# Kernel tuning notes

Hardware: AMD Instinct MI355X
Metric: run time of the kernel (lower is better)

Reference implementation:

```python
import jax, jax.numpy as jnp
import numpy as np

N = 8192
IN_DIM = 1024
HID = 64
N_CLASS = 40
N_LAYERS = 4  # N_LAYERS-1 hidden GraphConvolutions + 1 output layer


def _row_normalize(a):
    return a / jnp.clip(a.sum(axis=1, keepdims=True), 1e-6)


def setup_inputs() -> dict:
    key = jax.random.key(0)
    ks = jax.random.split(key, 10)
    x = jax.random.normal(ks[0], (N, IN_DIM), dtype=jnp.float32)
    # symmetric-ish normalized dense adjacency surrogates
    adj1 = _row_normalize(jax.random.uniform(ks[1], (N, N), dtype=jnp.float32))
    adj2 = _row_normalize(jax.random.uniform(ks[2], (N, N), dtype=jnp.float32))
    s_in = 1.0 / np.sqrt(IN_DIM)
    s_h = 1.0 / np.sqrt(HID)
    fc1_W = jax.random.uniform(ks[3], (IN_DIM, HID), minval=-s_in, maxval=s_in)
    fc1_b = jnp.zeros((HID,), jnp.float32)
    W_h = jax.random.uniform(ks[4], (N_LAYERS - 1, HID, HID), minval=-s_h, maxval=s_h)
    b_h = jnp.zeros((N_LAYERS - 1, HID), jnp.float32)
    W_out = jax.random.uniform(ks[5], (HID, N_CLASS), minval=-s_h, maxval=s_h)
    b_out = jnp.zeros((N_CLASS,), jnp.float32)
    return {"x": x, "adj1": adj1, "adj2": adj2, "fc1_W": fc1_W, "fc1_b": fc1_b,
            "W_h": W_h, "b_h": b_h, "W_out": W_out, "b_out": b_out}


def reference(x, adj1, adj2, fc1_W, fc1_b, W_h, b_h, W_out, b_out):
    # fc1 projection (dropout is identity in eval mode)
    h = x @ fc1_W + fc1_b  # [N, HID]
    # hidden GraphConvolution layers: aggregate, bias, residual, relu
    for i in range(W_h.shape[0]):
        h = jax.nn.relu(adj1 @ (h @ W_h[i]) + b_h[i] + h)
    # final layer: no residual
    out = jax.nn.relu(adj1 @ (h @ W_out) + b_out)  # [N, N_CLASS]
    return out
```

## Files before the change

kernel.cpp:

```cpp
#include <hip/hip_runtime.h>
#include <hip/hip_bf16.h>

typedef __attribute__((ext_vector_type(8))) short short8;
typedef __attribute__((ext_vector_type(4))) float f32x4;

#define NROWS 8192
#define BK 256
#define MTILE 128
#define SK 8

__device__ inline short f2bf(float f) {
  union { float f; unsigned u; } v; v.f = f;
  unsigned r = v.u + 0x7FFFu + ((v.u >> 16) & 1u);
  return (short)(r >> 16);
}

__global__ __launch_bounds__(256) void convert_adj_kernel(
    const float* __restrict__ A, short* __restrict__ AB) {
  const size_t total = (size_t)NROWS * NROWS;
  size_t i0 = ((size_t)blockIdx.x * 256 + threadIdx.x) * 8;
  size_t stride = (size_t)gridDim.x * 256 * 8;
  for (size_t i = i0; i < total; i += stride) {
    f32x4 a = __builtin_nontemporal_load((const f32x4*)(A + i));
    f32x4 b = __builtin_nontemporal_load((const f32x4*)(A + i + 4));
    short8 o;
    o[0] = f2bf(a.x); o[1] = f2bf(a.y); o[2] = f2bf(a.z); o[3] = f2bf(a.w);
    o[4] = f2bf(b.x); o[5] = f2bf(b.y); o[6] = f2bf(b.z); o[7] = f2bf(b.w);
    *(short8*)(AB + i) = o;
  }
}

__global__ __launch_bounds__(256) void convert_w_kernel(
    const float* __restrict__ W, short* __restrict__ WT, int K, int N) {
  int gid = blockIdx.x * 256 + threadIdx.x;
  if (gid >= K * N) return;
  int n = gid / K, k = gid - n * K;
  WT[gid] = f2bf(W[(size_t)k * N + n]);
}

__global__ __launch_bounds__(256) void small_t_kernel(
    const float* __restrict__ H, const float* __restrict__ W,
    short* __restrict__ tT, int Nout, int ldw) {
  __shared__ float Ws[64][64];
  int tid = threadIdx.x;
  for (int i = tid; i < 64 * 64; i += 256) {
    int j = i >> 6, n = i & 63;
    Ws[j][n] = (n < Nout) ? W[j * ldw + n] : 0.0f;
  }
  __syncthreads();
  int gid = blockIdx.x * 256 + tid;
  int m = gid >> 2;
  int nq = (gid & 3) << 4;
  const float* hrow = H + (size_t)m * 64;
  float hr[64];
#pragma unroll
  for (int j = 0; j < 64; j += 4) {
    f32x4 v = *(const f32x4*)(hrow + j);
    hr[j] = v.x; hr[j + 1] = v.y; hr[j + 2] = v.z; hr[j + 3] = v.w;
  }
#pragma unroll
  for (int ni = 0; ni < 16; ++ni) {
    int n = nq + ni;
    float acc = 0.0f;
#pragma unroll
    for (int j = 0; j < 64; ++j) acc += hr[j] * Ws[j][n];
    tT[(size_t)n * NROWS + m] = f2bf(acc);
  }
}

__global__ __launch_bounds__(256, 2) void gemm_bf16_lds2(
    const short* __restrict__ AB, const short* __restrict__ BT,
    float* __restrict__ P) {
  __shared__ short Bs[2][64][BK + 8];
  int tid = threadIdx.x;
  int w = tid >> 6, l = tid & 63;
  int l15 = l & 15, kg = l >> 4;
  int m_base = blockIdx.x * MTILE;
  int wrow = m_base + w * 32;
  const short* A0 = AB + (size_t)(wrow + l15) * NROWS;
  const short* A1 = AB + (size_t)(wrow + 16 + l15) * NROWS;
  const int KCH = NROWS / SK;
  const int NST = KCH / BK;
  int k0 = blockIdx.y * KCH;
  f32x4 acc[2][4];
#pragma unroll
  for (int rt = 0; rt < 2; ++rt)
#pragma unroll
    for (int ct = 0; ct < 4; ++ct) acc[rt][ct] = (f32x4){0, 0, 0, 0};

  short8 st[8];
#pragma unroll
  for (int j = 0; j < 8; ++j) {
    int slot = tid + 256 * j;
    int r = slot >> 5, c = (slot & 31) << 3;
    st[j] = *(const short8*)(BT + (size_t)r * NROWS + k0 + c);
  }
#pragma unroll
  for (int j = 0; j < 8; ++j) {
    int slot = tid + 256 * j;
    int r = slot >> 5, c = (slot & 31) << 3;
    *(short8*)&Bs[0][r][c] = st[j];
  }
  __syncthreads();

  for (int t = 0; t < NST; ++t) {
    int cur = t & 1;
    if (t + 1 < NST) {
      int ks = k0 + (t + 1) * BK;
#pragma unroll
      for (int j = 0; j < 8; ++j) {
        int slot = tid + 256 * j;
        int r = slot >> 5, c = (slot & 31) << 3;
        st[j] = *(const short8*)(BT + (size_t)r * NROWS + ks + c);
      }
    }
    int ks = k0 + t * BK;
#pragma unroll
    for (int k = 0; k < BK; k += 64) {
      short8 a[2][2], b[2][4];
#pragma unroll
      for (int u = 0; u < 2; ++u) {
        int kk = k + u * 32 + kg * 8;
        a[u][0] = *(const short8*)(A0 + ks + kk);
        a[u][1] = *(const short8*)(A1 + ks + kk);
        b[u][0] = *(const short8*)&Bs[cur][l15 +  0][kk];
        b[u][1] = *(const short8*)&Bs[cur][l15 + 16][kk];
        b[u][2] = *(const short8*)&Bs[cur][l15 + 32][kk];
        b[u][3] = *(const short8*)&Bs[cur][l15 + 48][kk];
      }
#pragma unroll
      for (int u = 0; u < 2; ++u)
#pragma unroll
        for (int ct = 0; ct < 4; ++ct) {
          acc[0][ct] = __builtin_amdgcn_mfma_f32_16x16x32_bf16(a[u][0], b[u][ct], acc[0][ct], 0, 0, 0);
          acc[1][ct] = __builtin_amdgcn_mfma_f32_16x16x32_bf16(a[u][1], b[u][ct], acc[1][ct], 0, 0, 0);
        }
    }
    __syncthreads();
    if (t + 1 < NST) {
#pragma unroll
      for (int j = 0; j < 8; ++j) {
        int slot = tid + 256 * j;
        int r = slot >> 5, c = (slot & 31) << 3;
        *(short8*)&Bs[cur ^ 1][r][c] = st[j];
      }
      __syncthreads();
    }
  }

  float* Pb = P + (size_t)blockIdx.y * (NROWS * 64);
#pragma unroll
  for (int rt = 0; rt < 2; ++rt)
#pragma unroll
    for (int r = 0; r < 4; ++r) {
      size_t base = (size_t)(wrow + rt * 16 + kg * 4 + r) * 64 + l15;
#pragma unroll
      for (int ct = 0; ct < 4; ++ct) Pb[base + 16 * ct] = acc[rt][ct][r];
    }
}

__global__ __launch_bounds__(256, 2) void gemm_a32_u2(
    const float* __restrict__ A, const short* __restrict__ BT,
    float* __restrict__ P, int K, int splitk) {
  int w = threadIdx.x >> 6;
  int l = threadIdx.x & 63;
  int l15 = l & 15, kg = l >> 4;
  int m_base = blockIdx.x * 64 + w * 16;
  const float* Arow = A + (size_t)(m_base + l15) * K;
  const short* Br = BT + (size_t)l15 * K;
  int kchunk = K / splitk;
  int k0 = blockIdx.y * kchunk;
  f32x4 acc[4] = {{0,0,0,0},{0,0,0,0},{0,0,0,0},{0,0,0,0}};
  for (int k = k0; k < k0 + kchunk; k += 64) {
    f32x4 a32[2][2];
    short8 b[2][4];
#pragma unroll
    for (int u = 0; u < 2; ++u) {
      int kk = k + u * 32 + kg * 8;
      a32[u][0] = __builtin_nontemporal_load((const f32x4*)(Arow + kk));
      a32[u][1] = __builtin_nontemporal_load((const f32x4*)(Arow + kk + 4));
      b[u][0] = *(const short8*)(Br + kk);
      b[u][1] = *(const short8*)(Br + (size_t)16 * K + kk);
      b[u][2] = *(const short8*)(Br + (size_t)32 * K + kk);
      b[u][3] = *(const short8*)(Br + (size_t)48 * K + kk);
    }
#pragma unroll
    for (int u = 0; u < 2; ++u) {
      short8 af;
      af[0] = f2bf(a32[u][0].x); af[1] = f2bf(a32[u][0].y);
      af[2] = f2bf(a32[u][0].z); af[3] = f2bf(a32[u][0].w);
      af[4] = f2bf(a32[u][1].x); af[5] = f2bf(a32[u][1].y);
      af[6] = f2bf(a32[u][1].z); af[7] = f2bf(a32[u][1].w);
#pragma unroll
      for (int t = 0; t < 4; ++t)
        acc[t] = __builtin_amdgcn_mfma_f32_16x16x32_bf16(af, b[u][t], acc[t], 0, 0, 0);
    }
  }
  float* Pb = P + (size_t)blockIdx.y * (NROWS * 64);
  int mr = m_base + kg * 4;
#pragma unroll
  for (int r = 0; r < 4; ++r) {
    size_t base = (size_t)(mr + r) * 64 + l15;
#pragma unroll
    for (int t = 0; t < 4; ++t) Pb[base + 16 * t] = acc[t][r];
  }
}

__global__ __launch_bounds__(256) void reduce4_kernel(
    const float* __restrict__ P, const float* __restrict__ bias,
    const float* __restrict__ Hres, float* __restrict__ Hout,
    float* __restrict__ Out, int mode, int splitk) {
  int gid = blockIdx.x * 256 + threadIdx.x;
  int e0 = gid * 4;
  int n = e0 & 63;
  f32x4 s = {0, 0, 0, 0};
  for (int sidx = 0; sidx < splitk; ++sidx)
    s += *(const f32x4*)(P + (size_t)sidx * (NROWS * 64) + e0);
  s += *(const f32x4*)(bias + n);
  if (mode == 0) {
    *(f32x4*)(Hout + e0) = s;
  } else if (mode == 1) {
    s += *(const f32x4*)(Hres + e0);
    s.x = s.x > 0.f ? s.x : 0.f; s.y = s.y > 0.f ? s.y : 0.f;
    s.z = s.z > 0.f ? s.z : 0.f; s.w = s.w > 0.f ? s.w : 0.f;
    *(f32x4*)(Hout + e0) = s;
  } else {
    if (n < 40) {
      int m = e0 >> 6;
      s.x = s.x > 0.f ? s.x : 0.f; s.y = s.y > 0.f ? s.y : 0.f;
      s.z = s.z > 0.f ? s.z : 0.f; s.w = s.w > 0.f ? s.w : 0.f;
      *(f32x4*)(Out + (size_t)m * 40 + n) = s;
    }
  }
}

extern "C" void kernel_launch(void* const* d_in, const int* in_sizes, int n_in,
                              void* d_out, int out_size, void* d_ws, size_t ws_size,
                              hipStream_t stream) {
  const float* x     = (const float*)d_in[0];
  const float* adj1  = (const float*)d_in[1];
  const float* fc1_W = (const float*)d_in[3];
  const float* fc1_b = (const float*)d_in[4];
  const float* W_h   = (const float*)d_in[5];
  const float* b_h   = (const float*)d_in[6];
  const float* W_out = (const float*)d_in[7];
  const float* b_out = (const float*)d_in[8];
  float* out = (float*)d_out;

  char* ws = (char*)d_ws;
  size_t off = 0;
  float* P   = (float*)(ws + off); off += (size_t)SK * NROWS * 64 * 4;
  float* h_a = (float*)(ws + off); off += (size_t)NROWS * 64 * 4;
  float* h_b = (float*)(ws + off); off += (size_t)NROWS * 64 * 4;
  short* tT  = (short*)(ws + off); off += (size_t)64 * NROWS * 2;
  short* WT  = (short*)(ws + off); off += (size_t)64 * 1024 * 2;
  size_t adjb_bytes = (size_t)NROWS * NROWS * 2;
  short* AB  = (ws_size - off >= adjb_bytes) ? (short*)(ws + off) : nullptr;

  const int RED_GRID = NROWS * 64 / 4 / 256;

  if (AB)
    convert_adj_kernel<<<2048, 256, 0, stream>>>(adj1, AB);

  convert_w_kernel<<<(1024 * 64 + 255) / 256, 256, 0, stream>>>(fc1_W, WT, 1024, 64);
  gemm_a32_u2<<<dim3(NROWS / 64, SK), 256, 0, stream>>>(x, WT, P, 1024, SK);
  reduce4_kernel<<<RED_GRID, 256, 0, stream>>>(P, fc1_b, nullptr, h_a, nullptr, 0, SK);

  float* hc = h_a; float* hn = h_b;
  for (int i = 0; i < 3; ++i) {
    small_t_kernel<<<NROWS * 4 / 256, 256, 0, stream>>>(hc, W_h + (size_t)i * 64 * 64, tT, 64, 64);
    if (AB)
      gemm_bf16_lds2<<<dim3(NROWS / MTILE, SK), 256, 0, stream>>>(AB, tT, P);
    else
      gemm_a32_u2<<<dim3(NROWS / 64, SK), 256, 0, stream>>>(adj1, tT, P, NROWS, SK);
    reduce4_kernel<<<RED_GRID, 256, 0, stream>>>(P, b_h + (size_t)i * 64, hc, hn, nullptr, 1, SK);
    float* t = hc; hc = hn; hn = t;
  }

  small_t_kernel<<<NROWS * 4 / 256, 256, 0, stream>>>(hc, W_out, tT, 40, 40);
  if (AB)
    gemm_bf16_lds2<<<dim3(NROWS / MTILE, SK), 256, 0, stream>>>(AB, tT, P);
  else
    gemm_a32_u2<<<dim3(NROWS / 64, SK), 256, 0, stream>>>(adj1, tT, P, NROWS, SK);
  reduce4_kernel<<<RED_GRID, 256, 0, stream>>>(P, b_out, nullptr, nullptr, out, 2, SK);
}
```

Baseline: 252.9 us.

## Fuse adjacency bf16 conversion into first aggregation GEMM and retile to 256 rows

Removes the separate fp32-to-bf16 adjacency conversion pass and folds it into the first aggregation GEMM. That kernel reads adj1 in fp32, converts it in registers, writes the bf16 copy for later layers and uses it directly in MFMA. Both adjacency GEMMs now use 256-row tiles, with each wave holding 4x4 accumulators, BK 128 and split-K of 16 for more A reuse per B tile. The trade-offs are more registers, a larger partial-sum buffer, and reduce kernels that now sum 16 partial slices instead of 8.

```diff
diff --git a/kernel.cpp b/kernel.cpp
--- a/kernel.cpp
+++ b/kernel.cpp
@@ -5,29 +5,15 @@
 typedef __attribute__((ext_vector_type(4))) float f32x4;
 
 #define NROWS 8192
-#define BK 256
-#define MTILE 128
-#define SK 8
+#define BK 128
+#define MTILE 256
+#define SKADJ 16
+#define SKFC 8
 
 __device__ inline short f2bf(float f) {
   union { float f; unsigned u; } v; v.f = f;
   unsigned r = v.u + 0x7FFFu + ((v.u >> 16) & 1u);
   return (short)(r >> 16);
-}
-
-__global__ __launch_bounds__(256) void convert_adj_kernel(
-    const float* __restrict__ A, short* __restrict__ AB) {
-  const size_t total = (size_t)NROWS * NROWS;
-  size_t i0 = ((size_t)blockIdx.x * 256 + threadIdx.x) * 8;
-  size_t stride = (size_t)gridDim.x * 256 * 8;
-  for (size_t i = i0; i < total; i += stride) {
-    f32x4 a = __builtin_nontemporal_load((const f32x4*)(A + i));
-    f32x4 b = __builtin_nontemporal_load((const f32x4*)(A + i + 4));
-    short8 o;
-    o[0] = f2bf(a.x); o[1] = f2bf(a.y); o[2] = f2bf(a.z); o[3] = f2bf(a.w);
-    o[4] = f2bf(b.x); o[5] = f2bf(b.y); o[6] = f2bf(b.z); o[7] = f2bf(b.w);
-    *(short8*)(AB + i) = o;
-  }
 }
 
 __global__ __launch_bounds__(256) void convert_w_kernel(
@@ -68,37 +54,39 @@
   }
 }
 
-__global__ __launch_bounds__(256, 2) void gemm_bf16_lds2(
+
+__global__ __launch_bounds__(256, 2) void gemm_bf16_r4(
     const short* __restrict__ AB, const short* __restrict__ BT,
     float* __restrict__ P) {
   __shared__ short Bs[2][64][BK + 8];
   int tid = threadIdx.x;
   int w = tid >> 6, l = tid & 63;
   int l15 = l & 15, kg = l >> 4;
-  int m_base = blockIdx.x * MTILE;
-  int wrow = m_base + w * 32;
-  const short* A0 = AB + (size_t)(wrow + l15) * NROWS;
+  int wrow = blockIdx.x * MTILE + w * 64;
+  const short* A0 = AB + (size_t)(wrow +  0 + l15) * NROWS;
   const short* A1 = AB + (size_t)(wrow + 16 + l15) * NROWS;
-  const int KCH = NROWS / SK;
+  const short* A2 = AB + (size_t)(wrow + 32 + l15) * NROWS;
+  const short* A3 = AB + (size_t)(wrow + 48 + l15) * NROWS;
+  const int KCH = NROWS / SKADJ;
   const int NST = KCH / BK;
   int k0 = blockIdx.y * KCH;
-  f32x4 acc[2][4];
-#pragma unroll
-  for (int rt = 0; rt < 2; ++rt)
+  f32x4 acc[4][4];
+#pragma unroll
+  for (int rt = 0; rt < 4; ++rt)
 #pragma unroll
     for (int ct = 0; ct < 4; ++ct) acc[rt][ct] = (f32x4){0, 0, 0, 0};
 
-  short8 st[8];
-#pragma unroll
-  for (int j = 0; j < 8; ++j) {
+  short8 st[4];
+#pragma unroll
+  for (int j = 0; j < 4; ++j) {
     int slot = tid + 256 * j;
-    int r = slot >> 5, c = (slot & 31) << 3;
+    int r = slot >> 4, c = (slot & 15) << 3;
     st[j] = *(const short8*)(BT + (size_t)r * NROWS + k0 + c);
   }
 #pragma unroll
-  for (int j = 0; j < 8; ++j) {
+  for (int j = 0; j < 4; ++j) {
     int slot = tid + 256 * j;
-    int r = slot >> 5, c = (slot & 31) << 3;
+    int r = slot >> 4, c = (slot & 15) << 3;
     *(short8*)&Bs[0][r][c] = st[j];
   }
   __syncthreads();
@@ -108,40 +96,50 @@
     if (t + 1 < NST) {
       int ks = k0 + (t + 1) * BK;
 #pragma unroll
-      for (int j = 0; j < 8; ++j) {
+      for (int j = 0; j < 4; ++j) {
         int slot = tid + 256 * j;
-        int r = slot >> 5, c = (slot & 31) << 3;
+        int r = slot >> 4, c = (slot & 15) << 3;
         st[j] = *(const short8*)(BT + (size_t)r * NROWS + ks + c);
       }
     }
     int ks = k0 + t * BK;
 #pragma unroll
     for (int k = 0; k < BK; k += 64) {
-      short8 a[2][2], b[2][4];
 #pragma unroll
       for (int u = 0; u < 2; ++u) {
         int kk = k + u * 32 + kg * 8;
-        a[u][0] = *(const short8*)(A0 + ks + kk);
-        a[u][1] = *(const short8*)(A1 + ks + kk);
-        b[u][0] = *(const short8*)&Bs[cur][l15 +  0][kk];
-        b[u][1] = *(const short8*)&Bs[cur][l15 + 16][kk];
-        b[u][2] = *(const short8*)&Bs[cur][l15 + 32][kk];
-        b[u][3] = *(const short8*)&Bs[cur][l15 + 48][kk];
-      }
-#pragma unroll
-      for (int u = 0; u < 2; ++u)
-#pragma unroll
-        for (int ct = 0; ct < 4; ++ct) {
-          acc[0][ct] = __builtin_amdgcn_mfma_f32_16x16x32_bf16(a[u][0], b[u][ct], acc[0][ct], 0, 0, 0);
-          acc[1][ct] = __builtin_amdgcn_mfma_f32_16x16x32_bf16(a[u][1], b[u][ct], acc[1][ct], 0, 0, 0);
-        }
+        short8 a0 = *(const short8*)(A0 + ks + kk);
+        short8 a1 = *(const short8*)(A1 + ks + kk);
+        short8 a2 = *(const short8*)(A2 + ks + kk);
+        short8 a3 = *(const short8*)(A3 + ks + kk);
+        short8 b0 = *(const short8*)&Bs[cur][l15 +  0][kk];
+        short8 b1 = *(const short8*)&Bs[cur][l15 + 16][kk];
+        short8 b2 = *(const short8*)&Bs[cur][l15 + 32][kk];
+        short8 b3 = *(const short8*)&Bs[cur][l15 + 48][kk];
+        acc[0][0] = __builtin_amdgcn_mfma_f32_16x16x32_bf16(a0, b0, acc[0][0], 0, 0, 0);
+        acc[0][1] = __builtin_amdgcn_mfma_f32_16x16x32_bf16(a0, b1, acc[0][1], 0, 0, 0);
+        acc[0][2] = __builtin_amdgcn_mfma_f32_16x16x32_bf16(a0, b2, acc[0][2], 0, 0, 0);
+        acc[0][3] = __builtin_amdgcn_mfma_f32_16x16x32_bf16(a0, b3, acc[0][3], 0, 0, 0);
+        acc[1][0] = __builtin_amdgcn_mfma_f32_16x16x32_bf16(a1, b0, acc[1][0], 0, 0, 0);
+        acc[1][1] = __builtin_amdgcn_mfma_f32_16x16x32_bf16(a1, b1, acc[1][1], 0, 0, 0);
+        acc[1][2] = __builtin_amdgcn_mfma_f32_16x16x32_bf16(a1, b2, acc[1][2], 0, 0, 0);
+        acc[1][3] = __builtin_amdgcn_mfma_f32_16x16x32_bf16(a1, b3, acc[1][3], 0, 0, 0);
+        acc[2][0] = __builtin_amdgcn_mfma_f32_16x16x32_bf16(a2, b0, acc[2][0], 0, 0, 0);
+        acc[2][1] = __builtin_amdgcn_mfma_f32_16x16x32_bf16(a2, b1, acc[2][1], 0, 0, 0);
+        acc[2][2] = __builtin_amdgcn_mfma_f32_16x16x32_bf16(a2, b2, acc[2][2], 0, 0, 0);
+        acc[2][3] = __builtin_amdgcn_mfma_f32_16x16x32_bf16(a2, b3, acc[2][3], 0, 0, 0);
+        acc[3][0] = __builtin_amdgcn_mfma_f32_16x16x32_bf16(a3, b0, acc[3][0], 0, 0, 0);
+        acc[3][1] = __builtin_amdgcn_mfma_f32_16x16x32_bf16(a3, b1, acc[3][1], 0, 0, 0);
+        acc[3][2] = __builtin_amdgcn_mfma_f32_16x16x32_bf16(a3, b2, acc[3][2], 0, 0, 0);
+        acc[3][3] = __builtin_amdgcn_mfma_f32_16x16x32_bf16(a3, b3, acc[3][3], 0, 0, 0);
+      }
     }
     __syncthreads();
     if (t + 1 < NST) {
 #pragma unroll
-      for (int j = 0; j < 8; ++j) {
+      for (int j = 0; j < 4; ++j) {
         int slot = tid + 256 * j;
-        int r = slot >> 5, c = (slot & 31) << 3;
+        int r = slot >> 4, c = (slot & 15) << 3;
         *(short8*)&Bs[cur ^ 1][r][c] = st[j];
       }
       __syncthreads();
@@ -150,7 +148,121 @@
 
   float* Pb = P + (size_t)blockIdx.y * (NROWS * 64);
 #pragma unroll
-  for (int rt = 0; rt < 2; ++rt)
+  for (int rt = 0; rt < 4; ++rt)
+#pragma unroll
+    for (int r = 0; r < 4; ++r) {
+      size_t base = (size_t)(wrow + rt * 16 + kg * 4 + r) * 64 + l15;
+#pragma unroll
+      for (int ct = 0; ct < 4; ++ct) Pb[base + 16 * ct] = acc[rt][ct][r];
+    }
+}
+
+__global__ __launch_bounds__(256, 2) void gemm_fusedcvt_r4(
+    const float* __restrict__ A, const short* __restrict__ BT,
+    float* __restrict__ P, short* __restrict__ AB) {
+  __shared__ short Bs[2][64][BK + 8];
+  int tid = threadIdx.x;
+  int w = tid >> 6, l = tid & 63;
+  int l15 = l & 15, kg = l >> 4;
+  int wrow = blockIdx.x * MTILE + w * 64;
+  const float* F0 = A + (size_t)(wrow +  0 + l15) * NROWS;
+  const float* F1 = A + (size_t)(wrow + 16 + l15) * NROWS;
+  const float* F2 = A + (size_t)(wrow + 32 + l15) * NROWS;
+  const float* F3 = A + (size_t)(wrow + 48 + l15) * NROWS;
+  short* S0 = AB + (size_t)(wrow +  0 + l15) * NROWS;
+  short* S1 = AB + (size_t)(wrow + 16 + l15) * NROWS;
+  short* S2 = AB + (size_t)(wrow + 32 + l15) * NROWS;
+  short* S3 = AB + (size_t)(wrow + 48 + l15) * NROWS;
+  const int KCH = NROWS / SKADJ;
+  const int NST = KCH / BK;
+  int k0 = blockIdx.y * KCH;
+  f32x4 acc[4][4];
+#pragma unroll
+  for (int rt = 0; rt < 4; ++rt)
+#pragma unroll
+    for (int ct = 0; ct < 4; ++ct) acc[rt][ct] = (f32x4){0, 0, 0, 0};
+
+  short8 st[4];
+#pragma unroll
+  for (int j = 0; j < 4; ++j) {
+    int slot = tid + 256 * j;
+    int r = slot >> 4, c = (slot & 15) << 3;
+    st[j] = *(const short8*)(BT + (size_t)r * NROWS + k0 + c);
+  }
+#pragma unroll
+  for (int j = 0; j < 4; ++j) {
+    int slot = tid + 256 * j;
+    int r = slot >> 4, c = (slot & 15) << 3;
+    *(short8*)&Bs[0][r][c] = st[j];
+  }
+  __syncthreads();
+
+  for (int t = 0; t < NST; ++t) {
+    int cur = t & 1;
+    if (t + 1 < NST) {
+      int ks = k0 + (t + 1) * BK;
+#pragma unroll
+      for (int j = 0; j < 4; ++j) {
+        int slot = tid + 256 * j;
+        int r = slot >> 4, c = (slot & 15) << 3;
+        st[j] = *(const short8*)(BT + (size_t)r * NROWS + ks + c);
+      }
+    }
+    int ks = k0 + t * BK;
+#pragma unroll
+    for (int k = 0; k < BK; k += 64) {
+#pragma unroll
+      for (int u = 0; u < 2; ++u) {
+        int kk = k + u * 32 + kg * 8;
+        f32x4 f[4][2];
+        f[0][0] = __builtin_nontemporal_load((const f32x4*)(F0 + ks + kk));
+        f[0][1] = __builtin_nontemporal_load((const f32x4*)(F0 + ks + kk + 4));
+        f[1][0] = __builtin_nontemporal_load((const f32x4*)(F1 + ks + kk));
+        f[1][1] = __builtin_nontemporal_load((const f32x4*)(F1 + ks + kk + 4));
+        f[2][0] = __builtin_nontemporal_load((const f32x4*)(F2 + ks + kk));
+        f[2][1] = __builtin_nontemporal_load((const f32x4*)(F2 + ks + kk + 4));
+        f[3][0] = __builtin_nontemporal_load((const f32x4*)(F3 + ks + kk));
+        f[3][1] = __builtin_nontemporal_load((const f32x4*)(F3 + ks + kk + 4));
+        short8 a[4];
+#pragma unroll
+        for (int rt = 0; rt < 4; ++rt) {
+          a[rt][0] = f2bf(f[rt][0].x); a[rt][1] = f2bf(f[rt][0].y);
+          a[rt][2] = f2bf(f[rt][0].z); a[rt][3] = f2bf(f[rt][0].w);
+          a[rt][4] = f2bf(f[rt][1].x); a[rt][5] = f2bf(f[rt][1].y);
+          a[rt][6] = f2bf(f[rt][1].z); a[rt][7] = f2bf(f[rt][1].w);
+        }
+        *(short8*)(S0 + ks + kk) = a[0];
+        *(short8*)(S1 + ks + kk) = a[1];
+        *(short8*)(S2 + ks + kk) = a[2];
+        *(short8*)(S3 + ks + kk) = a[3];
+        short8 b0 = *(const short8*)&Bs[cur][l15 +  0][kk];
+        short8 b1 = *(const short8*)&Bs[cur][l15 + 16][kk];
+        short8 b2 = *(const short8*)&Bs[cur][l15 + 32][kk];
+        short8 b3 = *(const short8*)&Bs[cur][l15 + 48][kk];
+#pragma unroll
+        for (int rt = 0; rt < 4; ++rt) {
+          acc[rt][0] = __builtin_amdgcn_mfma_f32_16x16x32_bf16(a[rt], b0, acc[rt][0], 0, 0, 0);
+          acc[rt][1] = __builtin_amdgcn_mfma_f32_16x16x32_bf16(a[rt], b1, acc[rt][1], 0, 0, 0);
+          acc[rt][2] = __builtin_amdgcn_mfma_f32_16x16x32_bf16(a[rt], b2, acc[rt][2], 0, 0, 0);
+          acc[rt][3] = __builtin_amdgcn_mfma_f32_16x16x32_bf16(a[rt], b3, acc[rt][3], 0, 0, 0);
+        }
+      }
+    }
+    __syncthreads();
+    if (t + 1 < NST) {
+#pragma unroll
+      for (int j = 0; j < 4; ++j) {
+        int slot = tid + 256 * j;
+        int r = slot >> 4, c = (slot & 15) << 3;
+        *(short8*)&Bs[cur ^ 1][r][c] = st[j];
+      }
+      __syncthreads();
+    }
+  }
+
+  float* Pb = P + (size_t)blockIdx.y * (NROWS * 64);
+#pragma unroll
+  for (int rt = 0; rt < 4; ++rt)
 #pragma unroll
     for (int r = 0; r < 4; ++r) {
       size_t base = (size_t)(wrow + rt * 16 + kg * 4 + r) * 64 + l15;
@@ -249,7 +361,7 @@
 
   char* ws = (char*)d_ws;
   size_t off = 0;
-  float* P   = (float*)(ws + off); off += (size_t)SK * NROWS * 64 * 4;
+  float* P   = (float*)(ws + off); off += (size_t)SKADJ * NROWS * 64 * 4;
   float* h_a = (float*)(ws + off); off += (size_t)NROWS * 64 * 4;
   float* h_b = (float*)(ws + off); off += (size_t)NROWS * 64 * 4;
   short* tT  = (short*)(ws + off); off += (size_t)64 * NROWS * 2;
@@ -259,28 +371,29 @@
 
   const int RED_GRID = NROWS * 64 / 4 / 256;
 
-  if (AB)
-    convert_adj_kernel<<<2048, 256, 0, stream>>>(adj1, AB);
-
   convert_w_kernel<<<(1024 * 64 + 255) / 256, 256, 0, stream>>>(fc1_W, WT, 1024, 64);
-  gemm_a32_u2<<<dim3(NROWS / 64, SK), 256, 0, stream>>>(x, WT, P, 1024, SK);
-  reduce4_kernel<<<RED_GRID, 256, 0, stream>>>(P, fc1_b, nullptr, h_a, nullptr, 0, SK);
+  gemm_a32_u2<<<dim3(NROWS / 64, SKFC), 256, 0, stream>>>(x, WT, P, 1024, SKFC);
+  reduce4_kernel<<<RED_GRID, 256, 0, stream>>>(P, fc1_b, nullptr, h_a, nullptr, 0, SKFC);
 
   float* hc = h_a; float* hn = h_b;
   for (int i = 0; i < 3; ++i) {
     small_t_kernel<<<NROWS * 4 / 256, 256, 0, stream>>>(hc, W_h + (size_t)i * 64 * 64, tT, 64, 64);
-    if (AB)
-      gemm_bf16_lds2<<<dim3(NROWS / MTILE, SK), 256, 0, stream>>>(AB, tT, P);
-    else
-      gemm_a32_u2<<<dim3(NROWS / 64, SK), 256, 0, stream>>>(adj1, tT, P, NROWS, SK);
-    reduce4_kernel<<<RED_GRID, 256, 0, stream>>>(P, b_h + (size_t)i * 64, hc, hn, nullptr, 1, SK);
+    if (AB) {
+      if (i == 0)
+        gemm_fusedcvt_r4<<<dim3(NROWS / MTILE, SKADJ), 256, 0, stream>>>(adj1, tT, P, AB);
+      else
+        gemm_bf16_r4<<<dim3(NROWS / MTILE, SKADJ), 256, 0, stream>>>(AB, tT, P);
+    } else {
+      gemm_a32_u2<<<dim3(NROWS / 64, SKADJ), 256, 0, stream>>>(adj1, tT, P, NROWS, SKADJ);
+    }
+    reduce4_kernel<<<RED_GRID, 256, 0, stream>>>(P, b_h + (size_t)i * 64, hc, hn, nullptr, 1, SKADJ);
     float* t = hc; hc = hn; hn = t;
   }
 
   small_t_kernel<<<NROWS * 4 / 256, 256, 0, stream>>>(hc, W_out, tT, 40, 40);
   if (AB)
-    gemm_bf16_lds2<<<dim3(NROWS / MTILE, SK), 256, 0, stream>>>(AB, tT, P);
+    gemm_bf16_r4<<<dim3(NROWS / MTILE, SKADJ), 256, 0, stream>>>(AB, tT, P);
   else
-    gemm_a32_u2<<<dim3(NROWS / 64, SK), 256, 0, stream>>>(adj1, tT, P, NROWS, SK);
-  reduce4_kernel<<<RED_GRID, 256, 0, stream>>>(P, b_out, nullptr, nullptr, out, 2, SK);
-}
+    gemm_a32_u2<<<dim3(NROWS / 64, SKADJ), 256, 0, stream>>>(adj1, tT, P, NROWS, SKADJ);
+  reduce4_kernel<<<RED_GRID, 256, 0, stream>>>(P, b_out, nullptr, nullptr, out, 2, SKADJ);
+}
```

Result: slower. 274.5 us (+8.5%).

## Enlarge adjacency GEMM to 64-row warp tiles, bf16 fc1 path, split-K 16

Applied to the files above, without the earlier changes.

The adjacency GEMM now has each warp cover 64 rows, with 4x4 MFMA tiles and 256-row blocks, so every LDS B fragment is reused across four A row tiles. Split-K rises to 16 to keep the grid large with the bigger tiles, which doubles the partial-sum traffic through the reduce kernels. The input x is also converted to bf16 so the fc1 projection can run on the same templated bf16 GEMM. The extra conversion pass and the higher register pressure from 64 accumulators per lane are the tradeoffs.

```diff
diff --git a/kernel.cpp b/kernel.cpp
--- a/kernel.cpp
+++ b/kernel.cpp
@@ -5,9 +5,9 @@
 typedef __attribute__((ext_vector_type(4))) float f32x4;
 
 #define NROWS 8192
-#define BK 256
-#define MTILE 128
-#define SK 8
+#define MTILE 256
+#define SKADJ 16
+#define SKFC 8
 
 __device__ inline short f2bf(float f) {
   union { float f; unsigned u; } v; v.f = f;
@@ -15,9 +15,8 @@
   return (short)(r >> 16);
 }
 
-__global__ __launch_bounds__(256) void convert_adj_kernel(
-    const float* __restrict__ A, short* __restrict__ AB) {
-  const size_t total = (size_t)NROWS * NROWS;
+__global__ __launch_bounds__(256) void convert_f32_kernel(
+    const float* __restrict__ A, short* __restrict__ O, size_t total) {
   size_t i0 = ((size_t)blockIdx.x * 256 + threadIdx.x) * 8;
   size_t stride = (size_t)gridDim.x * 256 * 8;
   for (size_t i = i0; i < total; i += stride) {
@@ -26,7 +25,7 @@
     short8 o;
     o[0] = f2bf(a.x); o[1] = f2bf(a.y); o[2] = f2bf(a.z); o[3] = f2bf(a.w);
     o[4] = f2bf(b.x); o[5] = f2bf(b.y); o[6] = f2bf(b.z); o[7] = f2bf(b.w);
-    *(short8*)(AB + i) = o;
+    *(short8*)(O + i) = o;
   }
 }
 
@@ -68,37 +67,40 @@
   }
 }
 
-__global__ __launch_bounds__(256, 2) void gemm_bf16_lds2(
-    const short* __restrict__ AB, const short* __restrict__ BT,
-    float* __restrict__ P) {
-  __shared__ short Bs[2][64][BK + 8];
+template <int TBK>
+__global__ __launch_bounds__(256, 2) void gemm_r4(
+    const short* __restrict__ A, const short* __restrict__ BT,
+    float* __restrict__ P, int K, int kchunk) {
+  __shared__ short Bs[2][64][TBK + 8];
+  constexpr int SLOTS = TBK / 8;
+  constexpr int JITER = 64 * SLOTS / 256;
   int tid = threadIdx.x;
   int w = tid >> 6, l = tid & 63;
   int l15 = l & 15, kg = l >> 4;
-  int m_base = blockIdx.x * MTILE;
-  int wrow = m_base + w * 32;
-  const short* A0 = AB + (size_t)(wrow + l15) * NROWS;
-  const short* A1 = AB + (size_t)(wrow + 16 + l15) * NROWS;
-  const int KCH = NROWS / SK;
-  const int NST = KCH / BK;
-  int k0 = blockIdx.y * KCH;
-  f32x4 acc[2][4];
-#pragma unroll
-  for (int rt = 0; rt < 2; ++rt)
+  int wrow = blockIdx.x * MTILE + w * 64;
+  const short* A0 = A + (size_t)(wrow +  0 + l15) * K;
+  const short* A1 = A + (size_t)(wrow + 16 + l15) * K;
+  const short* A2 = A + (size_t)(wrow + 32 + l15) * K;
+  const short* A3 = A + (size_t)(wrow + 48 + l15) * K;
+  const int NST = kchunk / TBK;
+  int k0 = blockIdx.y * kchunk;
+  f32x4 acc[4][4];
+#pragma unroll
+  for (int rt = 0; rt < 4; ++rt)
 #pragma unroll
     for (int ct = 0; ct < 4; ++ct) acc[rt][ct] = (f32x4){0, 0, 0, 0};
 
-  short8 st[8];
-#pragma unroll
-  for (int j = 0; j < 8; ++j) {
+  short8 st[JITER];
+#pragma unroll
+  for (int j = 0; j < JITER; ++j) {
     int slot = tid + 256 * j;
-    int r = slot >> 5, c = (slot & 31) << 3;
-    st[j] = *(const short8*)(BT + (size_t)r * NROWS + k0 + c);
-  }
-#pragma unroll
-  for (int j = 0; j < 8; ++j) {
+    int r = slot / SLOTS, c = (slot % SLOTS) * 8;
+    st[j] = *(const short8*)(BT + (size_t)r * K + k0 + c);
+  }
+#pragma unroll
+  for (int j = 0; j < JITER; ++j) {
     int slot = tid + 256 * j;
-    int r = slot >> 5, c = (slot & 31) << 3;
+    int r = slot / SLOTS, c = (slot % SLOTS) * 8;
     *(short8*)&Bs[0][r][c] = st[j];
   }
   __syncthreads();
@@ -106,42 +108,49 @@
   for (int t = 0; t < NST; ++t) {
     int cur = t & 1;
     if (t + 1 < NST) {
-      int ks = k0 + (t + 1) * BK;
-#pragma unroll
-      for (int j = 0; j < 8; ++j) {
+      int ks = k0 + (t + 1) * TBK;
+#pragma unroll
+      for (int j = 0; j < JITER; ++j) {
         int slot = tid + 256 * j;
-        int r = slot >> 5, c = (slot & 31) << 3;
-        st[j] = *(const short8*)(BT + (size_t)r * NROWS + ks + c);
+        int r = slot / SLOTS, c = (slot % SLOTS) * 8;
+        st[j] = *(const short8*)(BT + (size_t)r * K + ks + c);
       }
     }
-    int ks = k0 + t * BK;
-#pragma unroll
-    for (int k = 0; k < BK; k += 64) {
-      short8 a[2][2], b[2][4];
-#pragma unroll
-      for (int u = 0; u < 2; ++u) {
-        int kk = k + u * 32 + kg * 8;
-        a[u][0] = *(const short8*)(A0 + ks + kk);
-        a[u][1] = *(const short8*)(A1 + ks + kk);
-        b[u][0] = *(const short8*)&Bs[cur][l15 +  0][kk];
-        b[u][1] = *(const short8*)&Bs[cur][l15 + 16][kk];
-        b[u][2] = *(const short8*)&Bs[cur][l15 + 32][kk];
-        b[u][3] = *(const short8*)&Bs[cur][l15 + 48][kk];
-      }
-#pragma unroll
-      for (int u = 0; u < 2; ++u)
-#pragma unroll
-        for (int ct = 0; ct < 4; ++ct) {
-          acc[0][ct] = __builtin_amdgcn_mfma_f32_16x16x32_bf16(a[u][0], b[u][ct], acc[0][ct], 0, 0, 0);
-          acc[1][ct] = __builtin_amdgcn_mfma_f32_16x16x32_bf16(a[u][1], b[u][ct], acc[1][ct], 0, 0, 0);
-        }
+    int ks = k0 + t * TBK;
+#pragma unroll
+    for (int k = 0; k < TBK; k += 32) {
+      int kk = k + kg * 8;
+      short8 a0 = *(const short8*)(A0 + ks + kk);
+      short8 a1 = *(const short8*)(A1 + ks + kk);
+      short8 a2 = *(const short8*)(A2 + ks + kk);
+      short8 a3 = *(const short8*)(A3 + ks + kk);
+      short8 b0 = *(const short8*)&Bs[cur][l15 +  0][kk];
+      short8 b1 = *(const short8*)&Bs[cur][l15 + 16][kk];
+      short8 b2 = *(const short8*)&Bs[cur][l15 + 32][kk];
+      short8 b3 = *(const short8*)&Bs[cur][l15 + 48][kk];
+      acc[0][0] = __builtin_amdgcn_mfma_f32_16x16x32_bf16(a0, b0, acc[0][0], 0, 0, 0);
+      acc[0][1] = __builtin_amdgcn_mfma_f32_16x16x32_bf16(a0, b1, acc[0][1], 0, 0, 0);
+      acc[0][2] = __builtin_amdgcn_mfma_f32_16x16x32_bf16(a0, b2, acc[0][2], 0, 0, 0);
+      acc[0][3] = __builtin_amdgcn_mfma_f32_16x16x32_bf16(a0, b3, acc[0][3], 0, 0, 0);
+      acc[1][0] = __builtin_amdgcn_mfma_f32_16x16x32_bf16(a1, b0, acc[1][0], 0, 0, 0);
+      acc[1][1] = __builtin_amdgcn_mfma_f32_16x16x32_bf16(a1, b1, acc[1][1], 0, 0, 0);
+      acc[1][2] = __builtin_amdgcn_mfma_f32_16x16x32_bf16(a1, b2, acc[1][2], 0, 0, 0);
+      acc[1][3] = __builtin_amdgcn_mfma_f32_16x16x32_bf16(a1, b3, acc[1][3], 0, 0, 0);
+      acc[2][0] = __builtin_amdgcn_mfma_f32_16x16x32_bf16(a2, b0, acc[2][0], 0, 0, 0);
+      acc[2][1] = __builtin_amdgcn_mfma_f32_16x16x32_bf16(a2, b1, acc[2][1], 0, 0, 0);
+      acc[2][2] = __builtin_amdgcn_mfma_f32_16x16x32_bf16(a2, b2, acc[2][2], 0, 0, 0);
+      acc[2][3] = __builtin_amdgcn_mfma_f32_16x16x32_bf16(a2, b3, acc[2][3], 0, 0, 0);
+      acc[3][0] = __builtin_amdgcn_mfma_f32_16x16x32_bf16(a3, b0, acc[3][0], 0, 0, 0);
+      acc[3][1] = __builtin_amdgcn_mfma_f32_16x16x32_bf16(a3, b1, acc[3][1], 0, 0, 0);
+      acc[3][2] = __builtin_amdgcn_mfma_f32_16x16x32_bf16(a3, b2, acc[3][2], 0, 0, 0);
+      acc[3][3] = __builtin_amdgcn_mfma_f32_16x16x32_bf16(a3, b3, acc[3][3], 0, 0, 0);
     }
     __syncthreads();
     if (t + 1 < NST) {
 #pragma unroll
-      for (int j = 0; j < 8; ++j) {
+      for (int j = 0; j < JITER; ++j) {
         int slot = tid + 256 * j;
-        int r = slot >> 5, c = (slot & 31) << 3;
+        int r = slot / SLOTS, c = (slot % SLOTS) * 8;
         *(short8*)&Bs[cur ^ 1][r][c] = st[j];
       }
       __syncthreads();
@@ -150,7 +159,7 @@
 
   float* Pb = P + (size_t)blockIdx.y * (NROWS * 64);
 #pragma unroll
-  for (int rt = 0; rt < 2; ++rt)
+  for (int rt = 0; rt < 4; ++rt)
 #pragma unroll
     for (int r = 0; r < 4; ++r) {
       size_t base = (size_t)(wrow + rt * 16 + kg * 4 + r) * 64 + l15;
@@ -249,38 +258,46 @@
 
   char* ws = (char*)d_ws;
   size_t off = 0;
-  float* P   = (float*)(ws + off); off += (size_t)SK * NROWS * 64 * 4;
+  float* P   = (float*)(ws + off); off += (size_t)SKADJ * NROWS * 64 * 4;
   float* h_a = (float*)(ws + off); off += (size_t)NROWS * 64 * 4;
   float* h_b = (float*)(ws + off); off += (size_t)NROWS * 64 * 4;
   short* tT  = (short*)(ws + off); off += (size_t)64 * NROWS * 2;
   short* WT  = (short*)(ws + off); off += (size_t)64 * 1024 * 2;
   size_t adjb_bytes = (size_t)NROWS * NROWS * 2;
   short* AB  = (ws_size - off >= adjb_bytes) ? (short*)(ws + off) : nullptr;
+  if (AB) off += adjb_bytes;
+  size_t xb_bytes = (size_t)NROWS * 1024 * 2;
+  short* XB  = (ws_size - off >= xb_bytes) ? (short*)(ws + off) : nullptr;
 
   const int RED_GRID = NROWS * 64 / 4 / 256;
 
   if (AB)
-    convert_adj_kernel<<<2048, 256, 0, stream>>>(adj1, AB);
+    convert_f32_kernel<<<2048, 256, 0, stream>>>(adj1, AB, (size_t)NROWS * NROWS);
+  if (XB)
+    convert_f32_kernel<<<1024, 256, 0, stream>>>(x, XB, (size_t)NROWS * 1024);
 
   convert_w_kernel<<<(1024 * 64 + 255) / 256, 256, 0, stream>>>(fc1_W, WT, 1024, 64);
-  gemm_a32_u2<<<dim3(NROWS / 64, SK), 256, 0, stream>>>(x, WT, P, 1024, SK);
-  reduce4_kernel<<<RED_GRID, 256, 0, stream>>>(P, fc1_b, nullptr, h_a, nullptr, 0, SK);
+  if (XB)
+    gemm_r4<128><<<dim3(NROWS / MTILE, SKFC), 256, 0, stream>>>(XB, WT, P, 1024, 1024 / SKFC);
+  else
+    gemm_a32_u2<<<dim3(NROWS / 64, SKFC), 256, 0, stream>>>(x, WT, P, 1024, SKFC);
+  reduce4_kernel<<<RED_GRID, 256, 0, stream>>>(P, fc1_b, nullptr, h_a, nullptr, 0, SKFC);
 
   float* hc = h_a; float* hn = h_b;
   for (int i = 0; i < 3; ++i) {
     small_t_kernel<<<NROWS * 4 / 256, 256, 0, stream>>>(hc, W_h + (size_t)i * 64 * 64, tT, 64, 64);
     if (AB)
-      gemm_bf16_lds2<<<dim3(NROWS / MTILE, SK), 256, 0, stream>>>(AB, tT, P);
+      gemm_r4<256><<<dim3(NROWS / MTILE, SKADJ), 256, 0, stream>>>(AB, tT, P, NROWS, NROWS / SKADJ);
     else
-      gemm_a32_u2<<<dim3(NROWS / 64, SK), 256, 0, stream>>>(adj1, tT, P, NROWS, SK);
-    reduce4_kernel<<<RED_GRID, 256, 0, stream>>>(P, b_h + (size_t)i * 64, hc, hn, nullptr, 1, SK);
+      gemm_a32_u2<<<dim3(NROWS / 64, SKADJ), 256, 0, stream>>>(adj1, tT, P, NROWS, SKADJ);
+    reduce4_kernel<<<RED_GRID, 256, 0, stream>>>(P, b_h + (size_t)i * 64, hc, hn, nullptr, 1, SKADJ);
     float* t = hc; hc = hn; hn = t;
   }
 
   small_t_kernel<<<NROWS * 4 / 256, 256, 0, stream>>>(hc, W_out, tT, 40, 40);
   if (AB)
-    gemm_bf16_lds2<<<dim3(NROWS / MTILE, SK), 256, 0, stream>>>(AB, tT, P);
+    gemm_r4<256><<<dim3(NROWS / MTILE, SKADJ), 256, 0, stream>>>(AB, tT, P, NROWS, NROWS / SKADJ);
   else
-    gemm_a32_u2<<<dim3(NROWS / 64, SK), 256, 0, stream>>>(adj1, tT, P, NROWS, SK);
-  reduce4_kernel<<<RED_GRID, 256, 0, stream>>>(P, b_out, nullptr, nullptr, out, 2, SK);
-}
+    gemm_a32_u2<<<dim3(NROWS / 64, SKADJ), 256, 0, stream>>>(adj1, tT, P, NROWS, SKADJ);
+  reduce4_kernel<<<RED_GRID, 256, 0, stream>>>(P, b_out, nullptr, nullptr, out, 2, SKADJ);
+}
```

Result: slower. 268.3 us (+6.1%).
